# Performance work log

Measured on AMD Instinct MI355X. Metric: run time of the kernel, lower is better.

The kernel has to match this reference:

```python
import jax, jax.numpy as jnp
import numpy as np

D_MODEL = 1024
D_OUT = 128  # output_embed_size (head dim)

def setup_inputs() -> dict:
    key = jax.random.key(0)
    ks = jax.random.split(key, 4)
    x = jax.random.normal(ks[0], (2, 4096, D_MODEL), dtype=jnp.float32)
    # weights mimic nn.init.normal_(std=0.02), biases zero
    qW_w = 0.02 * jax.random.normal(ks[1], (D_OUT, D_MODEL), dtype=jnp.float32)
    kW_w = 0.02 * jax.random.normal(ks[2], (D_OUT, D_MODEL), dtype=jnp.float32)
    vW_w = 0.02 * jax.random.normal(ks[3], (D_OUT, D_MODEL), dtype=jnp.float32)
    zb = jnp.zeros((D_OUT,), dtype=jnp.float32)
    return {"x": x, "qW_w": qW_w, "qW_b": zb, "kW_w": kW_w, "kW_b": zb,
            "vW_w": vW_w, "vW_b": zb}

def reference(x, qW_w, qW_b, kW_w, kW_b, vW_w, vW_b):
    # Linear: y = x @ W^T + b
    Q = jnp.einsum('bsd,ed->bse', x, qW_w) + qW_b  # [B,S,E]
    K = jnp.einsum('bsd,ed->bse', x, kW_w) + kW_b
    V = jnp.einsum('bsd,ed->bse', x, vW_w) + vW_b
    scale = 1.0 / jnp.sqrt(jnp.float32(D_OUT))
    attention = jnp.einsum('bqe,bke->bqk', Q, K) * scale  # [B,S,S], NO softmax
    output = jnp.einsum('bqk,bke->bqe', attention, V)     # [B,S,E]
    return output
```

## Files before the change

kernel.cpp:

```cpp
#include <hip/hip_runtime.h>

#define SS 4096
#define DD 1024
#define EE 128
#define SCALE 0.08838834764831845f

typedef __bf16 bf16x8 __attribute__((ext_vector_type(8)));
typedef float  f32x4  __attribute__((ext_vector_type(4)));

__device__ __forceinline__ void gload16(const void* g, void* l) {
  __builtin_amdgcn_global_load_lds(
      (const __attribute__((address_space(1))) void*)g,
      (__attribute__((address_space(3))) void*)l, 16, 0, 0);
}

__global__ __launch_bounds__(256) void wcast_kernel(
    const float* __restrict__ qW, const float* __restrict__ kW,
    const float* __restrict__ vW, __bf16* __restrict__ Wb)
{
  const int m = blockIdx.y;
  const float* src = (m == 0) ? qW : (m == 1 ? kW : vW);
  const size_t o = ((size_t)blockIdx.x * 256 + threadIdx.x) * 8;
  float4 u0 = *(const float4*)&src[o];
  float4 u1 = *(const float4*)&src[o + 4];
  bf16x8 v = { (__bf16)u0.x, (__bf16)u0.y, (__bf16)u0.z, (__bf16)u0.w,
               (__bf16)u1.x, (__bf16)u1.y, (__bf16)u1.z, (__bf16)u1.w };
  *(bf16x8*)&Wb[(size_t)m * EE * DD + o] = v;
}

__global__ __launch_bounds__(256) void proj_kernel(
    const float* __restrict__ x, const __bf16* __restrict__ Wb,
    const float* __restrict__ qB, const float* __restrict__ kB,
    const float* __restrict__ vB,
    __bf16* __restrict__ Qbf, __bf16* __restrict__ KT, __bf16* __restrict__ VT)
{
  __shared__ __attribute__((aligned(16))) float  ldsA[2][64 * 64];
  __shared__ __attribute__((aligned(16))) __bf16 ldsB[2][64 * 64];

  const int tid  = threadIdx.x;
  const int w    = tid >> 6, lane = tid & 63;
  const int l15  = lane & 15, l4 = lane >> 4;
  const int wr   = w >> 1, wc = w & 1;

  const int id   = blockIdx.x;
  const int swz  = (id & 7) * 96 + (id >> 3);
  const int rt   = swz / 6, ct = swz % 6;
  const int row0 = rt * 64;
  const int g0   = ct * 64;

  const int aRow = lane >> 4;
  const int aPos = lane & 15;
  const int cE   = aPos ^ aRow;
  const int cO   = aPos ^ (4 | aRow);
  const float* gAe = x + (size_t)(row0 + w * 16 + aRow) * DD + cE * 4;
  const float* gAo = x + (size_t)(row0 + w * 16 + aRow) * DD + cO * 4;
  const int bRow = lane >> 3;
  const int cB   = (lane & 7) ^ bRow;
  const __bf16* gB = Wb + (size_t)(g0 + w * 16 + bRow) * DD + cB * 8;

  f32x4 acc[2][2] = {};

#define STAGE(P, T) {                                                        \
    const int k0_ = (T) * 64;                                                \
    gload16(gAe + k0_,                    &ldsA[P][(w * 16 +  0) * 64]);     \
    gload16(gAo + k0_ + (size_t) 4 * DD,  &ldsA[P][(w * 16 +  4) * 64]);     \
    gload16(gAe + k0_ + (size_t) 8 * DD,  &ldsA[P][(w * 16 +  8) * 64]);     \
    gload16(gAo + k0_ + (size_t)12 * DD,  &ldsA[P][(w * 16 + 12) * 64]);     \
    gload16(gB  + k0_,                    &ldsB[P][(w * 16 +  0) * 64]);     \
    gload16(gB  + k0_ + (size_t) 8 * DD,  &ldsB[P][(w * 16 +  8) * 64]);     }

#define CVT8(LO, HI) (bf16x8){ (__bf16)(LO)[0], (__bf16)(LO)[1],             \
    (__bf16)(LO)[2], (__bf16)(LO)[3], (__bf16)(HI)[0], (__bf16)(HI)[1],      \
    (__bf16)(HI)[2], (__bf16)(HI)[3] }

#define COMPUTE(P) {                                                         \
    const int rs7 = l15 & 7;                                                 \
    _Pragma("unroll") for (int ks = 0; ks < 2; ++ks) {                       \
      bf16x8 af[2], bq[2];                                                   \
      _Pragma("unroll") for (int m = 0; m < 2; ++m) {                        \
        const int row = wr * 32 + m * 16 + l15;                              \
        const int c0 = ks * 8 + l4 * 2;                                      \
        f32x4 lo = *(const f32x4*)&ldsA[P][row * 64 + (( c0      ^ rs7) << 2)]; \
        f32x4 hi = *(const f32x4*)&ldsA[P][row * 64 + (((c0 + 1) ^ rs7) << 2)]; \
        af[m] = CVT8(lo, hi);                                                \
      }                                                                      \
      _Pragma("unroll") for (int n = 0; n < 2; ++n) {                        \
        const int row = wc * 32 + n * 16 + l15;                              \
        bq[n] = *(const bf16x8*)&ldsB[P][row * 64 + (((ks*4 + l4) ^ rs7) << 3)]; \
      }                                                                      \
      acc[0][0] = __builtin_amdgcn_mfma_f32_16x16x32_bf16(af[0],bq[0],acc[0][0],0,0,0); \
      acc[0][1] = __builtin_amdgcn_mfma_f32_16x16x32_bf16(af[0],bq[1],acc[0][1],0,0,0); \
      acc[1][0] = __builtin_amdgcn_mfma_f32_16x16x32_bf16(af[1],bq[0],acc[1][0],0,0,0); \
      acc[1][1] = __builtin_amdgcn_mfma_f32_16x16x32_bf16(af[1],bq[1],acc[1][1],0,0,0); \
    } }

  STAGE(0, 0);
  __syncthreads();
  for (int t = 0; t < 15; ++t) {
    STAGE((t + 1) & 1, t + 1);
    COMPUTE(t & 1);
    __syncthreads();
  }
  COMPUTE(1);
  __syncthreads();
#undef STAGE
#undef CVT8
#undef COMPUTE

  const float* bias = (g0 < 128) ? qB : (g0 < 256 ? kB : vB);
  const int bofs = (g0 < 128) ? g0 : (g0 < 256 ? g0 - 128 : g0 - 256);

  if (ct < 2) {
    #pragma unroll
    for (int m = 0; m < 2; ++m)
      #pragma unroll
      for (int n = 0; n < 2; ++n) {
        const int col = wc * 32 + n * 16 + l15;
        const float bv = bias[bofs + col];
        #pragma unroll
        for (int r = 0; r < 4; ++r) {
          const int row = row0 + wr * 32 + m * 16 + l4 * 4 + r;
          Qbf[(size_t)row * EE + g0 + col] = (__bf16)(acc[m][n][r] + bv);
        }
      }
  } else {
    __bf16* Tb = (__bf16*)ldsA;
    #pragma unroll
    for (int m = 0; m < 2; ++m)
      #pragma unroll
      for (int n = 0; n < 2; ++n) {
        const int tc = wc * 32 + n * 16 + l15;
        const float bv = bias[bofs + tc];
        #pragma unroll
        for (int r = 0; r < 4; ++r) {
          const int rl = wr * 32 + m * 16 + l4 * 4 + r;
          Tb[tc * 64 + (((rl >> 3) ^ (tc & 7)) << 3) + (rl & 7)] =
              (__bf16)(acc[m][n][r] + bv);
        }
      }
    __syncthreads();
    const int col = tid >> 2, p2 = tid & 3;
    const int b = row0 >> 12, s0 = row0 & 4095;
    __bf16* dst = (ct < 4)
        ? &KT[((size_t)b * EE + (ct - 2) * 64 + col) * SS + s0]
        : &VT[((size_t)b * EE + (ct - 4) * 64 + col) * SS + s0];
    #pragma unroll
    for (int j = 0; j < 2; ++j) {
      const int ch = p2 * 2 + j;
      bf16x8 v = *(const bf16x8*)&Tb[col * 64 + ((ch ^ (col & 7)) << 3)];
      *(bf16x8*)&dst[ch * 8] = v;
    }
  }
}

__global__ __launch_bounds__(256) void ktv_kernel(
    const __bf16* __restrict__ KT, const __bf16* __restrict__ VT,
    float* __restrict__ part)
{
  const int c = blockIdx.x, b = blockIdx.y;
  const int tid = threadIdx.x;
  const int w = tid >> 6, lane = tid & 63;
  const int l15 = lane & 15, l4 = lane >> 4;
  const int s0 = c * 128;
  const __bf16* Kb = KT + (size_t)b * EE * SS;
  const __bf16* Vb = VT + (size_t)b * EE * SS;

  f32x4 acc[8][2] = {};
  #pragma unroll
  for (int ks = 0; ks < 4; ++ks) {
    const int s = s0 + ks * 32 + 8 * l4;
    bf16x8 bv[2];
    #pragma unroll
    for (int j = 0; j < 2; ++j)
      bv[j] = *(const bf16x8*)&Vb[(size_t)(w * 32 + j * 16 + l15) * SS + s];
    #pragma unroll
    for (int i = 0; i < 8; ++i) {
      bf16x8 av = *(const bf16x8*)&Kb[(size_t)(i * 16 + l15) * SS + s];
      acc[i][0] = __builtin_amdgcn_mfma_f32_16x16x32_bf16(av, bv[0], acc[i][0], 0, 0, 0);
      acc[i][1] = __builtin_amdgcn_mfma_f32_16x16x32_bf16(av, bv[1], acc[i][1], 0, 0, 0);
    }
  }
  float* P = part + (size_t)(b * 32 + c) * 16384;
  #pragma unroll
  for (int i = 0; i < 8; ++i)
    #pragma unroll
    for (int j = 0; j < 2; ++j)
      #pragma unroll
      for (int r = 0; r < 4; ++r) {
        int e = i * 16 + l4 * 4 + r;
        int f = w * 32 + j * 16 + l15;
        P[e * 128 + f] = acc[i][j][r];
      }
}

__global__ __launch_bounds__(256) void reduce_kernel(
    const float* __restrict__ part, __bf16* __restrict__ MT)
{
  const int b = blockIdx.y;
  const int e = blockIdx.x * 8 + (threadIdx.x >> 5);
  const int f4 = (threadIdx.x & 31) * 4;
  f32x4 s = {};
  for (int cc = 0; cc < 32; ++cc)
    s += *(const f32x4*)&part[(size_t)(b * 32 + cc) * 16384 + e * 128 + f4];
  #pragma unroll
  for (int i = 0; i < 4; ++i)
    MT[((size_t)b * EE + f4 + i) * EE + e] = (__bf16)(SCALE * s[i]);
}

__global__ __launch_bounds__(256) void qm_kernel(
    const __bf16* __restrict__ Qbf, const __bf16* __restrict__ MT,
    float* __restrict__ out)
{
  const int b = blockIdx.y;
  const int tid = threadIdx.x;
  const int w = tid >> 6, lane = tid & 63;
  const int l15 = lane & 15, l4 = lane >> 4;
  const int row0 = blockIdx.x * 64 + w * 16;
  const __bf16* Qb = Qbf + (size_t)b * SS * EE;
  const __bf16* Mb = MT + (size_t)b * EE * EE;

  f32x4 acc[8] = {};
  #pragma unroll
  for (int ks = 0; ks < 4; ++ks) {
    const int e = ks * 32 + 8 * l4;
    bf16x8 av = *(const bf16x8*)&Qb[(size_t)(row0 + l15) * EE + e];
    #pragma unroll
    for (int j = 0; j < 8; ++j) {
      bf16x8 bv = *(const bf16x8*)&Mb[(size_t)(j * 16 + l15) * EE + e];
      acc[j] = __builtin_amdgcn_mfma_f32_16x16x32_bf16(av, bv, acc[j], 0, 0, 0);
    }
  }
  #pragma unroll
  for (int j = 0; j < 8; ++j)
    #pragma unroll
    for (int r = 0; r < 4; ++r) {
      int srow = row0 + l4 * 4 + r;
      int f = j * 16 + l15;
      out[((size_t)b * SS + srow) * EE + f] = acc[j][r];
    }
}

extern "C" void kernel_launch(void* const* d_in, const int* in_sizes, int n_in,
                              void* d_out, int out_size, void* d_ws, size_t ws_size,
                              hipStream_t stream) {
  const float* x  = (const float*)d_in[0];
  const float* qW = (const float*)d_in[1];
  const float* qB = (const float*)d_in[2];
  const float* kW = (const float*)d_in[3];
  const float* kB = (const float*)d_in[4];
  const float* vW = (const float*)d_in[5];
  const float* vB = (const float*)d_in[6];
  float* out = (float*)d_out;

  char* base = (char*)d_ws;
  __bf16* Wb  = (__bf16*)(base);
  __bf16* Qbf = (__bf16*)(base + (1u  << 20));
  __bf16* KT  = (__bf16*)(base + (3u  << 20));
  __bf16* VT  = (__bf16*)(base + (5u  << 20));
  float*  part= (float*) (base + (7u  << 20));
  __bf16* MT  = (__bf16*)(base + (11u << 20));

  wcast_kernel <<<dim3(64, 3), 256, 0, stream>>>(qW, kW, vW, Wb);
  proj_kernel  <<<dim3(768),   256, 0, stream>>>(x, Wb, qB, kB, vB, Qbf, KT, VT);
  ktv_kernel   <<<dim3(32, 2), 256, 0, stream>>>(KT, VT, part);
  reduce_kernel<<<dim3(16, 2), 256, 0, stream>>>(part, MT);
  qm_kernel    <<<dim3(64, 2), 256, 0, stream>>>(Qbf, MT, out);
}
```

Measured before the change: 46.77 us.

## Widen projection tiles to 96 columns and increase parallelism of K^T V stages

The projection kernel now computes 64x96 output tiles over 512 blocks instead of 64x64 over 768, so each x tile is loaded and converted fewer times. The epilogue is generalised to handle tiles that mix Q columns with transposed K/V columns. The K^T V partial kernel is split across more blocks (64-row chunks of S and halves of the feature dimension), with a matching 64-way reduction and a smaller-block qm launch. The aim is to cut redundant reads of x and to fill more CUs in the small later kernels, at the cost of more partial-sum traffic and more divergent epilogue code.

```diff
diff --git a/kernel.cpp b/kernel.cpp
--- a/kernel.cpp
+++ b/kernel.cpp
@@ -35,7 +35,7 @@
     __bf16* __restrict__ Qbf, __bf16* __restrict__ KT, __bf16* __restrict__ VT)
 {
   __shared__ __attribute__((aligned(16))) float  ldsA[2][64 * 64];
-  __shared__ __attribute__((aligned(16))) __bf16 ldsB[2][64 * 64];
+  __shared__ __attribute__((aligned(16))) __bf16 ldsB[2][96 * 64];
 
   const int tid  = threadIdx.x;
   const int w    = tid >> 6, lane = tid & 63;
@@ -43,10 +43,10 @@
   const int wr   = w >> 1, wc = w & 1;
 
   const int id   = blockIdx.x;
-  const int swz  = (id & 7) * 96 + (id >> 3);
-  const int rt   = swz / 6, ct = swz % 6;
+  const int swz  = (id & 7) * 64 + (id >> 3);
+  const int rt   = swz >> 2, ct = swz & 3;
   const int row0 = rt * 64;
-  const int g0   = ct * 64;
+  const int g0   = ct * 96;
 
   const int aRow = lane >> 4;
   const int aPos = lane & 15;
@@ -56,9 +56,9 @@
   const float* gAo = x + (size_t)(row0 + w * 16 + aRow) * DD + cO * 4;
   const int bRow = lane >> 3;
   const int cB   = (lane & 7) ^ bRow;
-  const __bf16* gB = Wb + (size_t)(g0 + w * 16 + bRow) * DD + cB * 8;
-
-  f32x4 acc[2][2] = {};
+  const __bf16* gB = Wb + (size_t)(g0 + w * 24 + bRow) * DD + cB * 8;
+
+  f32x4 acc[2][3] = {};
 
 #define STAGE(P, T) {                                                        \
     const int k0_ = (T) * 64;                                                \
@@ -66,8 +66,9 @@
     gload16(gAo + k0_ + (size_t) 4 * DD,  &ldsA[P][(w * 16 +  4) * 64]);     \
     gload16(gAe + k0_ + (size_t) 8 * DD,  &ldsA[P][(w * 16 +  8) * 64]);     \
     gload16(gAo + k0_ + (size_t)12 * DD,  &ldsA[P][(w * 16 + 12) * 64]);     \
-    gload16(gB  + k0_,                    &ldsB[P][(w * 16 +  0) * 64]);     \
-    gload16(gB  + k0_ + (size_t) 8 * DD,  &ldsB[P][(w * 16 +  8) * 64]);     }
+    gload16(gB  + k0_,                    &ldsB[P][(w * 24 +  0) * 64]);     \
+    gload16(gB  + k0_ + (size_t) 8 * DD,  &ldsB[P][(w * 24 +  8) * 64]);     \
+    gload16(gB  + k0_ + (size_t)16 * DD,  &ldsB[P][(w * 24 + 16) * 64]);     }
 
 #define CVT8(LO, HI) (bf16x8){ (__bf16)(LO)[0], (__bf16)(LO)[1],             \
     (__bf16)(LO)[2], (__bf16)(LO)[3], (__bf16)(HI)[0], (__bf16)(HI)[1],      \
@@ -76,7 +77,7 @@
 #define COMPUTE(P) {                                                         \
     const int rs7 = l15 & 7;                                                 \
     _Pragma("unroll") for (int ks = 0; ks < 2; ++ks) {                       \
-      bf16x8 af[2], bq[2];                                                   \
+      bf16x8 af[2], bq[3];                                                   \
       _Pragma("unroll") for (int m = 0; m < 2; ++m) {                        \
         const int row = wr * 32 + m * 16 + l15;                              \
         const int c0 = ks * 8 + l4 * 2;                                      \
@@ -84,14 +85,14 @@
         f32x4 hi = *(const f32x4*)&ldsA[P][row * 64 + (((c0 + 1) ^ rs7) << 2)]; \
         af[m] = CVT8(lo, hi);                                                \
       }                                                                      \
-      _Pragma("unroll") for (int n = 0; n < 2; ++n) {                        \
-        const int row = wc * 32 + n * 16 + l15;                              \
+      _Pragma("unroll") for (int n = 0; n < 3; ++n) {                        \
+        const int row = wc * 48 + n * 16 + l15;                              \
         bq[n] = *(const bf16x8*)&ldsB[P][row * 64 + (((ks*4 + l4) ^ rs7) << 3)]; \
       }                                                                      \
-      acc[0][0] = __builtin_amdgcn_mfma_f32_16x16x32_bf16(af[0],bq[0],acc[0][0],0,0,0); \
-      acc[0][1] = __builtin_amdgcn_mfma_f32_16x16x32_bf16(af[0],bq[1],acc[0][1],0,0,0); \
-      acc[1][0] = __builtin_amdgcn_mfma_f32_16x16x32_bf16(af[1],bq[0],acc[1][0],0,0,0); \
-      acc[1][1] = __builtin_amdgcn_mfma_f32_16x16x32_bf16(af[1],bq[1],acc[1][1],0,0,0); \
+      _Pragma("unroll") for (int m = 0; m < 2; ++m)                          \
+        _Pragma("unroll") for (int n = 0; n < 3; ++n)                        \
+          acc[m][n] = __builtin_amdgcn_mfma_f32_16x16x32_bf16(               \
+              af[m], bq[n], acc[m][n], 0, 0, 0);                             \
     } }
 
   STAGE(0, 0);
@@ -107,30 +108,22 @@
 #undef CVT8
 #undef COMPUTE
 
-  const float* bias = (g0 < 128) ? qB : (g0 < 256 ? kB : vB);
-  const int bofs = (g0 < 128) ? g0 : (g0 < 256 ? g0 - 128 : g0 - 256);
-
-  if (ct < 2) {
-    #pragma unroll
-    for (int m = 0; m < 2; ++m)
-      #pragma unroll
-      for (int n = 0; n < 2; ++n) {
-        const int col = wc * 32 + n * 16 + l15;
-        const float bv = bias[bofs + col];
+  __bf16* Tb = (__bf16*)ldsA;
+  #pragma unroll
+  for (int m = 0; m < 2; ++m)
+    #pragma unroll
+    for (int n = 0; n < 3; ++n) {
+      const int colg = g0 + wc * 48 + n * 16 + l15;
+      if (colg < 128) {
+        const float bv = qB[colg];
         #pragma unroll
         for (int r = 0; r < 4; ++r) {
           const int row = row0 + wr * 32 + m * 16 + l4 * 4 + r;
-          Qbf[(size_t)row * EE + g0 + col] = (__bf16)(acc[m][n][r] + bv);
+          Qbf[(size_t)row * EE + colg] = (__bf16)(acc[m][n][r] + bv);
         }
-      }
-  } else {
-    __bf16* Tb = (__bf16*)ldsA;
-    #pragma unroll
-    for (int m = 0; m < 2; ++m)
-      #pragma unroll
-      for (int n = 0; n < 2; ++n) {
-        const int tc = wc * 32 + n * 16 + l15;
-        const float bv = bias[bofs + tc];
+      } else {
+        const float bv = (colg < 256) ? kB[colg - 128] : vB[colg - 256];
+        const int tc = wc * 48 + n * 16 + l15;
         #pragma unroll
         for (int r = 0; r < 4; ++r) {
           const int rl = wr * 32 + m * 16 + l4 * 4 + r;
@@ -138,17 +131,23 @@
               (__bf16)(acc[m][n][r] + bv);
         }
       }
-    __syncthreads();
-    const int col = tid >> 2, p2 = tid & 3;
-    const int b = row0 >> 12, s0 = row0 & 4095;
-    __bf16* dst = (ct < 4)
-        ? &KT[((size_t)b * EE + (ct - 2) * 64 + col) * SS + s0]
-        : &VT[((size_t)b * EE + (ct - 4) * 64 + col) * SS + s0];
-    #pragma unroll
-    for (int j = 0; j < 2; ++j) {
-      const int ch = p2 * 2 + j;
-      bf16x8 v = *(const bf16x8*)&Tb[col * 64 + ((ch ^ (col & 7)) << 3)];
-      *(bf16x8*)&dst[ch * 8] = v;
+    }
+  __syncthreads();
+  {
+    const int bb = row0 >> 12, s0v = row0 & 4095;
+    for (int idx = tid; idx < 96 * 4; idx += 256) {
+      const int tc = idx >> 2, p2 = idx & 3;
+      const int colg = g0 + tc;
+      if (colg >= 128) {
+        const int cl = colg & 127;
+        __bf16* dst = ((colg < 256) ? KT : VT) + ((size_t)bb * EE + cl) * SS + s0v;
+        #pragma unroll
+        for (int j = 0; j < 2; ++j) {
+          const int ch = p2 * 2 + j;
+          bf16x8 v = *(const bf16x8*)&Tb[tc * 64 + ((ch ^ (tc & 7)) << 3)];
+          *(bf16x8*)&dst[ch * 8] = v;
+        }
+      }
     }
   }
 }
@@ -157,57 +156,50 @@
     const __bf16* __restrict__ KT, const __bf16* __restrict__ VT,
     float* __restrict__ part)
 {
-  const int c = blockIdx.x, b = blockIdx.y;
+  const int c = blockIdx.x, fh = blockIdx.y, b = blockIdx.z;
   const int tid = threadIdx.x;
   const int w = tid >> 6, lane = tid & 63;
   const int l15 = lane & 15, l4 = lane >> 4;
-  const int s0 = c * 128;
+  const int s0 = c * 64;
+  const int fbase = fh * 64 + w * 16;
   const __bf16* Kb = KT + (size_t)b * EE * SS;
   const __bf16* Vb = VT + (size_t)b * EE * SS;
 
-  f32x4 acc[8][2] = {};
-  #pragma unroll
-  for (int ks = 0; ks < 4; ++ks) {
+  f32x4 acc[8] = {};
+  #pragma unroll
+  for (int ks = 0; ks < 2; ++ks) {
     const int s = s0 + ks * 32 + 8 * l4;
-    bf16x8 bv[2];
-    #pragma unroll
-    for (int j = 0; j < 2; ++j)
-      bv[j] = *(const bf16x8*)&Vb[(size_t)(w * 32 + j * 16 + l15) * SS + s];
+    bf16x8 bv = *(const bf16x8*)&Vb[(size_t)(fbase + l15) * SS + s];
     #pragma unroll
     for (int i = 0; i < 8; ++i) {
       bf16x8 av = *(const bf16x8*)&Kb[(size_t)(i * 16 + l15) * SS + s];
-      acc[i][0] = __builtin_amdgcn_mfma_f32_16x16x32_bf16(av, bv[0], acc[i][0], 0, 0, 0);
-      acc[i][1] = __builtin_amdgcn_mfma_f32_16x16x32_bf16(av, bv[1], acc[i][1], 0, 0, 0);
-    }
-  }
-  float* P = part + (size_t)(b * 32 + c) * 16384;
+      acc[i] = __builtin_amdgcn_mfma_f32_16x16x32_bf16(av, bv, acc[i], 0, 0, 0);
+    }
+  }
+  float* P = part + (size_t)(b * 64 + c) * 16384;
   #pragma unroll
   for (int i = 0; i < 8; ++i)
     #pragma unroll
-    for (int j = 0; j < 2; ++j)
-      #pragma unroll
-      for (int r = 0; r < 4; ++r) {
-        int e = i * 16 + l4 * 4 + r;
-        int f = w * 32 + j * 16 + l15;
-        P[e * 128 + f] = acc[i][j][r];
-      }
+    for (int r = 0; r < 4; ++r) {
+      int e = i * 16 + l4 * 4 + r;
+      int f = fbase + l15;
+      P[e * 128 + f] = acc[i][r];
+    }
 }
 
 __global__ __launch_bounds__(256) void reduce_kernel(
     const float* __restrict__ part, __bf16* __restrict__ MT)
 {
   const int b = blockIdx.y;
-  const int e = blockIdx.x * 8 + (threadIdx.x >> 5);
-  const int f4 = (threadIdx.x & 31) * 4;
-  f32x4 s = {};
-  for (int cc = 0; cc < 32; ++cc)
-    s += *(const f32x4*)&part[(size_t)(b * 32 + cc) * 16384 + e * 128 + f4];
-  #pragma unroll
-  for (int i = 0; i < 4; ++i)
-    MT[((size_t)b * EE + f4 + i) * EE + e] = (__bf16)(SCALE * s[i]);
-}
-
-__global__ __launch_bounds__(256) void qm_kernel(
+  const int e = blockIdx.x * 2 + (threadIdx.x >> 7);
+  const int f = threadIdx.x & 127;
+  float s = 0.f;
+  for (int cc = 0; cc < 64; ++cc)
+    s += part[(size_t)(b * 64 + cc) * 16384 + e * 128 + f];
+  MT[((size_t)b * EE + f) * EE + e] = (__bf16)(SCALE * s);
+}
+
+__global__ __launch_bounds__(128) void qm_kernel(
     const __bf16* __restrict__ Qbf, const __bf16* __restrict__ MT,
     float* __restrict__ out)
 {
@@ -215,7 +207,7 @@
   const int tid = threadIdx.x;
   const int w = tid >> 6, lane = tid & 63;
   const int l15 = lane & 15, l4 = lane >> 4;
-  const int row0 = blockIdx.x * 64 + w * 16;
+  const int row0 = blockIdx.x * 32 + w * 16;
   const __bf16* Qb = Qbf + (size_t)b * SS * EE;
   const __bf16* Mb = MT + (size_t)b * EE * EE;
 
@@ -258,11 +250,11 @@
   __bf16* KT  = (__bf16*)(base + (3u  << 20));
   __bf16* VT  = (__bf16*)(base + (5u  << 20));
   float*  part= (float*) (base + (7u  << 20));
-  __bf16* MT  = (__bf16*)(base + (11u << 20));
-
-  wcast_kernel <<<dim3(64, 3), 256, 0, stream>>>(qW, kW, vW, Wb);
-  proj_kernel  <<<dim3(768),   256, 0, stream>>>(x, Wb, qB, kB, vB, Qbf, KT, VT);
-  ktv_kernel   <<<dim3(32, 2), 256, 0, stream>>>(KT, VT, part);
-  reduce_kernel<<<dim3(16, 2), 256, 0, stream>>>(part, MT);
-  qm_kernel    <<<dim3(64, 2), 256, 0, stream>>>(Qbf, MT, out);
-}
+  __bf16* MT  = (__bf16*)(base + (15u << 20));
+
+  wcast_kernel <<<dim3(64, 3),    256, 0, stream>>>(qW, kW, vW, Wb);
+  proj_kernel  <<<dim3(512),      256, 0, stream>>>(x, Wb, qB, kB, vB, Qbf, KT, VT);
+  ktv_kernel   <<<dim3(64, 2, 2), 256, 0, stream>>>(KT, VT, part);
+  reduce_kernel<<<dim3(64, 2),    256, 0, stream>>>(part, MT);
+  qm_kernel    <<<dim3(128, 2),   128, 0, stream>>>(Qbf, MT, out);
+}
```

Measured after the change: 42.71 us. -8.7%, faster.

## Fuse weight cast into projection and widen grids of small downstream kernels

Applied to the files above, without the earlier changes.

Removes the separate weight-cast kernel. The projection kernel now loads fp32 weights into registers, converts them to bf16 and writes them to LDS inside its pipeline, and gains an occupancy hint in its launch bounds. The attention scale moves into the Q epilogue. The K^T·V, reduce and Q·M kernels are split into more, smaller blocks so more compute units are busy, at the cost of a larger partial-sum buffer and more reduction reads. This trades one launch and a staging buffer for register-staged weight loads and extra conversion work inside the main GEMM loop.

```diff
diff --git a/kernel.cpp b/kernel.cpp
--- a/kernel.cpp
+++ b/kernel.cpp
@@ -14,24 +14,11 @@
       (__attribute__((address_space(3))) void*)l, 16, 0, 0);
 }
 
-__global__ __launch_bounds__(256) void wcast_kernel(
-    const float* __restrict__ qW, const float* __restrict__ kW,
-    const float* __restrict__ vW, __bf16* __restrict__ Wb)
-{
-  const int m = blockIdx.y;
-  const float* src = (m == 0) ? qW : (m == 1 ? kW : vW);
-  const size_t o = ((size_t)blockIdx.x * 256 + threadIdx.x) * 8;
-  float4 u0 = *(const float4*)&src[o];
-  float4 u1 = *(const float4*)&src[o + 4];
-  bf16x8 v = { (__bf16)u0.x, (__bf16)u0.y, (__bf16)u0.z, (__bf16)u0.w,
-               (__bf16)u1.x, (__bf16)u1.y, (__bf16)u1.z, (__bf16)u1.w };
-  *(bf16x8*)&Wb[(size_t)m * EE * DD + o] = v;
-}
-
-__global__ __launch_bounds__(256) void proj_kernel(
-    const float* __restrict__ x, const __bf16* __restrict__ Wb,
-    const float* __restrict__ qB, const float* __restrict__ kB,
-    const float* __restrict__ vB,
+__global__ __launch_bounds__(256, 3) void proj_kernel(
+    const float* __restrict__ x,
+    const float* __restrict__ qW, const float* __restrict__ qB,
+    const float* __restrict__ kW, const float* __restrict__ kB,
+    const float* __restrict__ vW, const float* __restrict__ vB,
     __bf16* __restrict__ Qbf, __bf16* __restrict__ KT, __bf16* __restrict__ VT)
 {
   __shared__ __attribute__((aligned(16))) float  ldsA[2][64 * 64];
@@ -47,6 +34,10 @@
   const int rt   = swz / 6, ct = swz % 6;
   const int row0 = rt * 64;
   const int g0   = ct * 64;
+
+  const float* __restrict__ Wsel = (ct < 2) ? qW : (ct < 4 ? kW : vW);
+  const float* __restrict__ bias = (ct < 2) ? qB : (ct < 4 ? kB : vB);
+  const int bofs = (ct < 2) ? g0 : (ct < 4 ? g0 - 128 : g0 - 256);
 
   const int aRow = lane >> 4;
   const int aPos = lane & 15;
@@ -54,20 +45,36 @@
   const int cO   = aPos ^ (4 | aRow);
   const float* gAe = x + (size_t)(row0 + w * 16 + aRow) * DD + cE * 4;
   const float* gAo = x + (size_t)(row0 + w * 16 + aRow) * DD + cO * 4;
-  const int bRow = lane >> 3;
-  const int cB   = (lane & 7) ^ bRow;
-  const __bf16* gB = Wb + (size_t)(g0 + w * 16 + bRow) * DD + cB * 8;
+
+  const int brow = tid >> 2;
+  const int bseg = tid & 3;
+  const int brs  = brow & 7;
+  const float* gBW = Wsel + (size_t)(bofs + brow) * DD + bseg * 16;
 
   f32x4 acc[2][2] = {};
-
-#define STAGE(P, T) {                                                        \
+  f32x4 rB[4];
+
+#define BLOAD(T) {                                                           \
+    const float* g_ = gBW + (T) * 64;                                        \
+    rB[0] = *(const f32x4*)(g_);      rB[1] = *(const f32x4*)(g_ + 4);       \
+    rB[2] = *(const f32x4*)(g_ + 8);  rB[3] = *(const f32x4*)(g_ + 12); }
+
+#define BWRITE(P) {                                                          \
+    bf16x8 v0_ = { (__bf16)rB[0][0], (__bf16)rB[0][1], (__bf16)rB[0][2],     \
+                   (__bf16)rB[0][3], (__bf16)rB[1][0], (__bf16)rB[1][1],     \
+                   (__bf16)rB[1][2], (__bf16)rB[1][3] };                     \
+    bf16x8 v1_ = { (__bf16)rB[2][0], (__bf16)rB[2][1], (__bf16)rB[2][2],     \
+                   (__bf16)rB[2][3], (__bf16)rB[3][0], (__bf16)rB[3][1],     \
+                   (__bf16)rB[3][2], (__bf16)rB[3][3] };                     \
+    *(bf16x8*)&ldsB[P][brow * 64 + (((bseg * 2)     ^ brs) << 3)] = v0_;     \
+    *(bf16x8*)&ldsB[P][brow * 64 + (((bseg * 2 + 1) ^ brs) << 3)] = v1_; }
+
+#define ASTAGE(P, T) {                                                       \
     const int k0_ = (T) * 64;                                                \
     gload16(gAe + k0_,                    &ldsA[P][(w * 16 +  0) * 64]);     \
     gload16(gAo + k0_ + (size_t) 4 * DD,  &ldsA[P][(w * 16 +  4) * 64]);     \
     gload16(gAe + k0_ + (size_t) 8 * DD,  &ldsA[P][(w * 16 +  8) * 64]);     \
-    gload16(gAo + k0_ + (size_t)12 * DD,  &ldsA[P][(w * 16 + 12) * 64]);     \
-    gload16(gB  + k0_,                    &ldsB[P][(w * 16 +  0) * 64]);     \
-    gload16(gB  + k0_ + (size_t) 8 * DD,  &ldsB[P][(w * 16 +  8) * 64]);     }
+    gload16(gAo + k0_ + (size_t)12 * DD,  &ldsA[P][(w * 16 + 12) * 64]);     }
 
 #define CVT8(LO, HI) (bf16x8){ (__bf16)(LO)[0], (__bf16)(LO)[1],             \
     (__bf16)(LO)[2], (__bf16)(LO)[3], (__bf16)(HI)[0], (__bf16)(HI)[1],      \
@@ -94,21 +101,25 @@
       acc[1][1] = __builtin_amdgcn_mfma_f32_16x16x32_bf16(af[1],bq[1],acc[1][1],0,0,0); \
     } }
 
-  STAGE(0, 0);
+  BLOAD(0);
+  ASTAGE(0, 0);
+  BWRITE(0);
   __syncthreads();
   for (int t = 0; t < 15; ++t) {
-    STAGE((t + 1) & 1, t + 1);
-    COMPUTE(t & 1);
+    const int P = t & 1;
+    BLOAD(t + 1);
+    ASTAGE(P ^ 1, t + 1);
+    COMPUTE(P);
+    BWRITE(P ^ 1);
     __syncthreads();
   }
   COMPUTE(1);
   __syncthreads();
-#undef STAGE
+#undef BLOAD
+#undef BWRITE
+#undef ASTAGE
 #undef CVT8
 #undef COMPUTE
-
-  const float* bias = (g0 < 128) ? qB : (g0 < 256 ? kB : vB);
-  const int bofs = (g0 < 128) ? g0 : (g0 < 256 ? g0 - 128 : g0 - 256);
 
   if (ct < 2) {
     #pragma unroll
@@ -120,7 +131,8 @@
         #pragma unroll
         for (int r = 0; r < 4; ++r) {
           const int row = row0 + wr * 32 + m * 16 + l4 * 4 + r;
-          Qbf[(size_t)row * EE + g0 + col] = (__bf16)(acc[m][n][r] + bv);
+          Qbf[(size_t)row * EE + g0 + col] =
+              (__bf16)((acc[m][n][r] + bv) * SCALE);
         }
       }
   } else {
@@ -157,57 +169,50 @@
     const __bf16* __restrict__ KT, const __bf16* __restrict__ VT,
     float* __restrict__ part)
 {
-  const int c = blockIdx.x, b = blockIdx.y;
+  const int c = blockIdx.x, fh = blockIdx.y, b = blockIdx.z;
   const int tid = threadIdx.x;
   const int w = tid >> 6, lane = tid & 63;
   const int l15 = lane & 15, l4 = lane >> 4;
-  const int s0 = c * 128;
+  const int s0 = c * 64;
+  const int fbase = fh * 64 + w * 16;
   const __bf16* Kb = KT + (size_t)b * EE * SS;
   const __bf16* Vb = VT + (size_t)b * EE * SS;
 
-  f32x4 acc[8][2] = {};
-  #pragma unroll
-  for (int ks = 0; ks < 4; ++ks) {
+  f32x4 acc[8] = {};
+  #pragma unroll
+  for (int ks = 0; ks < 2; ++ks) {
     const int s = s0 + ks * 32 + 8 * l4;
-    bf16x8 bv[2];
-    #pragma unroll
-    for (int j = 0; j < 2; ++j)
-      bv[j] = *(const bf16x8*)&Vb[(size_t)(w * 32 + j * 16 + l15) * SS + s];
+    bf16x8 bv = *(const bf16x8*)&Vb[(size_t)(fbase + l15) * SS + s];
     #pragma unroll
     for (int i = 0; i < 8; ++i) {
       bf16x8 av = *(const bf16x8*)&Kb[(size_t)(i * 16 + l15) * SS + s];
-      acc[i][0] = __builtin_amdgcn_mfma_f32_16x16x32_bf16(av, bv[0], acc[i][0], 0, 0, 0);
-      acc[i][1] = __builtin_amdgcn_mfma_f32_16x16x32_bf16(av, bv[1], acc[i][1], 0, 0, 0);
-    }
-  }
-  float* P = part + (size_t)(b * 32 + c) * 16384;
+      acc[i] = __builtin_amdgcn_mfma_f32_16x16x32_bf16(av, bv, acc[i], 0, 0, 0);
+    }
+  }
+  float* P = part + (size_t)(b * 64 + c) * 16384;
   #pragma unroll
   for (int i = 0; i < 8; ++i)
     #pragma unroll
-    for (int j = 0; j < 2; ++j)
-      #pragma unroll
-      for (int r = 0; r < 4; ++r) {
-        int e = i * 16 + l4 * 4 + r;
-        int f = w * 32 + j * 16 + l15;
-        P[e * 128 + f] = acc[i][j][r];
-      }
+    for (int r = 0; r < 4; ++r) {
+      int e = i * 16 + l4 * 4 + r;
+      int f = fbase + l15;
+      P[e * 128 + f] = acc[i][r];
+    }
 }
 
 __global__ __launch_bounds__(256) void reduce_kernel(
     const float* __restrict__ part, __bf16* __restrict__ MT)
 {
   const int b = blockIdx.y;
-  const int e = blockIdx.x * 8 + (threadIdx.x >> 5);
-  const int f4 = (threadIdx.x & 31) * 4;
-  f32x4 s = {};
-  for (int cc = 0; cc < 32; ++cc)
-    s += *(const f32x4*)&part[(size_t)(b * 32 + cc) * 16384 + e * 128 + f4];
-  #pragma unroll
-  for (int i = 0; i < 4; ++i)
-    MT[((size_t)b * EE + f4 + i) * EE + e] = (__bf16)(SCALE * s[i]);
-}
-
-__global__ __launch_bounds__(256) void qm_kernel(
+  const int e = blockIdx.x * 2 + (threadIdx.x >> 7);
+  const int f = threadIdx.x & 127;
+  float s = 0.f;
+  for (int cc = 0; cc < 64; ++cc)
+    s += part[(size_t)(b * 64 + cc) * 16384 + e * 128 + f];
+  MT[((size_t)b * EE + f) * EE + e] = (__bf16)s;
+}
+
+__global__ __launch_bounds__(128) void qm_kernel(
     const __bf16* __restrict__ Qbf, const __bf16* __restrict__ MT,
     float* __restrict__ out)
 {
@@ -215,7 +220,7 @@
   const int tid = threadIdx.x;
   const int w = tid >> 6, lane = tid & 63;
   const int l15 = lane & 15, l4 = lane >> 4;
-  const int row0 = blockIdx.x * 64 + w * 16;
+  const int row0 = blockIdx.x * 32 + w * 16;
   const __bf16* Qb = Qbf + (size_t)b * SS * EE;
   const __bf16* Mb = MT + (size_t)b * EE * EE;
 
@@ -253,16 +258,15 @@
   float* out = (float*)d_out;
 
   char* base = (char*)d_ws;
-  __bf16* Wb  = (__bf16*)(base);
-  __bf16* Qbf = (__bf16*)(base + (1u  << 20));
-  __bf16* KT  = (__bf16*)(base + (3u  << 20));
-  __bf16* VT  = (__bf16*)(base + (5u  << 20));
-  float*  part= (float*) (base + (7u  << 20));
-  __bf16* MT  = (__bf16*)(base + (11u << 20));
-
-  wcast_kernel <<<dim3(64, 3), 256, 0, stream>>>(qW, kW, vW, Wb);
-  proj_kernel  <<<dim3(768),   256, 0, stream>>>(x, Wb, qB, kB, vB, Qbf, KT, VT);
-  ktv_kernel   <<<dim3(32, 2), 256, 0, stream>>>(KT, VT, part);
-  reduce_kernel<<<dim3(16, 2), 256, 0, stream>>>(part, MT);
-  qm_kernel    <<<dim3(64, 2), 256, 0, stream>>>(Qbf, MT, out);
-}
+  __bf16* Qbf = (__bf16*)(base);
+  __bf16* KT  = (__bf16*)(base + (2u  << 20));
+  __bf16* VT  = (__bf16*)(base + (4u  << 20));
+  float*  part= (float*) (base + (6u  << 20));
+  __bf16* MT  = (__bf16*)(base + (14u << 20));
+
+  proj_kernel  <<<dim3(768),      256, 0, stream>>>(x, qW, qB, kW, kB, vW, vB,
+                                                    Qbf, KT, VT);
+  ktv_kernel   <<<dim3(64, 2, 2), 256, 0, stream>>>(KT, VT, part);
+  reduce_kernel<<<dim3(64, 2),    256, 0, stream>>>(part, MT);
+  qm_kernel    <<<dim3(128, 2),   128, 0, stream>>>(Qbf, MT, out);
+}
```

New measurement: 43.22 us. 7.6% less time.
